# Optimization experiments

Hardware: AMD Instinct MI355X
Metric: run time of the kernel (lower is better)

The kernel has to match this reference:

```python
import jax, jax.numpy as jnp
import numpy as np

H = 16  # hidden size = time_slot(=32) / 2
G = 3 * H  # gate dim (r|z|n), torch gate order


def _gru_dir(x, Wi, Wh, bi, bh, reverse):
    """Single-direction GRU over time. x: [B,T,F]; Wi:[3H,F]; Wh:[3H,H]."""
    xp = jnp.einsum('btf,gf->btg', x, Wi) + bi  # [B,T,3H] input projections, all steps at once
    if reverse:
        xp = xp[:, ::-1]
    xp_t = jnp.swapaxes(xp, 0, 1)  # [T,B,3H]
    h0 = jnp.zeros((x.shape[0], H), x.dtype)

    def step(h, g_x):
        g_h = h @ Wh.T + bh  # [B,3H]
        r = jax.nn.sigmoid(g_x[:, :H] + g_h[:, :H])
        z = jax.nn.sigmoid(g_x[:, H:2 * H] + g_h[:, H:2 * H])
        n = jnp.tanh(g_x[:, 2 * H:] + r * g_h[:, 2 * H:])
        h_new = (1.0 - z) * n + z * h
        return h_new, h_new

    _, ys = jax.lax.scan(step, h0, xp_t)
    ys = jnp.swapaxes(ys, 0, 1)  # [B,T,H]
    if reverse:
        ys = ys[:, ::-1]
    return ys


def _bigru(x, Wi, Wh, bi, bh):
    """Bidirectional GRU layer; params indexed [dir(2), ...]."""
    fwd = _gru_dir(x, Wi[0], Wh[0], bi[0], bh[0], False)
    bwd = _gru_dir(x, Wi[1], Wh[1], bi[1], bh[1], True)
    return jnp.concatenate([fwd, bwd], axis=-1)  # [B,T,2H]


def setup_inputs() -> dict:
    key = jax.random.key(0)
    ks = jax.random.split(key, 12)
    B, T, F_IN, DEPTH, NCLS = 16384, 64, 3, 5, 4
    s = 0.25  # ~1/sqrt(H) torch init scale
    return {
        'x': jax.random.normal(ks[0], (B, T, F_IN), jnp.float32),
        # GRU1: 1 layer, 2 directions, input 3
        'Wi1': jax.random.normal(ks[1], (2, G, F_IN), jnp.float32) * s,
        'Wh1': jax.random.normal(ks[2], (2, G, H), jnp.float32) * s,
        'bi1': jax.random.normal(ks[3], (2, G), jnp.float32) * s,
        'bh1': jax.random.normal(ks[4], (2, G), jnp.float32) * s,
        # GRU5: 5 layers, 2 directions, input 2H=32 every layer
        'Wi5': jax.random.normal(ks[5], (DEPTH, 2, G, 2 * H), jnp.float32) * s,
        'Wh5': jax.random.normal(ks[6], (DEPTH, 2, G, H), jnp.float32) * s,
        'bi5': jax.random.normal(ks[7], (DEPTH, 2, G), jnp.float32) * s,
        'bh5': jax.random.normal(ks[8], (DEPTH, 2, G), jnp.float32) * s,
        # classifier Linear(2H -> num_class)
        'Wc': jax.random.normal(ks[9], (NCLS, 2 * H), jnp.float32) * s,
        'bc': jax.random.normal(ks[10], (NCLS,), jnp.float32) * s,
    }


def reference(x, Wi1, Wh1, bi1, bh1, Wi5, Wh5, bi5, bh5, Wc, bc):
    y = _bigru(x, Wi1, Wh1, bi1, bh1)  # [B,T,2H]
    for l in range(Wi5.shape[0]):  # 5 stacked bi-GRU layers
        y = _bigru(y, Wi5[l], Wh5[l], bi5[l], bh5[l])
    logits = jnp.einsum('btd,cd->btc', y, Wc) + bc  # [B,T,num_class]
    return jax.nn.softmax(logits, axis=2)
```

## Files before the change

### kernel.cpp

```cpp
#include <hip/hip_runtime.h>

#define T 64
#define F_IN 3
#define H 16
#define G 48
#define D2 32
#define DEPTH 5
#define NCLS 4
#define L2E 1.44269504f

#define YST 32
#define YSB 2048
#define HZ_ZOFF 64

typedef _Float16 half8 __attribute__((ext_vector_type(8)));
typedef float f32x4v __attribute__((ext_vector_type(4)));

__device__ __forceinline__ float fexp2(float x) { return __builtin_amdgcn_exp2f(x); }
__device__ __forceinline__ float frcp(float x)  { return __builtin_amdgcn_rcpf(x); }

__global__ __launch_bounds__(64, 3) void bigru_all(
    const float* __restrict__ x,
    const float* __restrict__ Wi1, const float* __restrict__ Wh1,
    const float* __restrict__ bi1, const float* __restrict__ bh1,
    const float* __restrict__ Wi5, const float* __restrict__ Wh5,
    const float* __restrict__ bi5, const float* __restrict__ bh5,
    const float* __restrict__ Wc,  const float* __restrict__ bc,
    float* __restrict__ out)
{
    __shared__ __align__(16) _Float16 yb[2 * YSB];
    __shared__ __align__(16) _Float16 hzb[80];
    __shared__ __align__(16) float xls[512];

    const int lane = threadIdx.x;
    const int j15  = lane & 15;
    const int quad = lane >> 4;
    const int lb   = quad & 1;
    const int dir  = quad >> 1;
    const bool isf = (dir == 0);

    hzb[lane] = (_Float16)0.0f;
    if (lane < 16) hzb[64 + lane] = (_Float16)0.0f;

    {
        const float* xg0 = x + (size_t)blockIdx.x * (2 * T * F_IN);
        #pragma unroll
        for (int k = 0; k < 2; ++k) {
            int idx = lane + 64 * k;
            float a0 = xg0[3 * idx], a1 = xg0[3 * idx + 1], a2 = xg0[3 * idx + 2];
            float4 v; v.x = a0; v.y = a1; v.z = a2; v.w = 0.0f;
            *(float4*)(xls + 4 * idx) = v;
        }
    }

    const int  job_a  = j15 >> 2;
    const bool avalid = ((j15 >> 3) == 0) ? (quad < 2) : (quad >= 2);
    const _Float16* aptr = hzb + (avalid ? (job_a * 16 + (quad & 1) * 8) : HZ_ZOFF);

    const int ystep = isf ? YST : -YST;
    const f32x4v zC = {0.f, 0.f, 0.f, 0.f};
    const int klo = (quad & 1) * 8;
    const int bdir = (quad < 2) ? 0 : 1;

    float hj;
    half8 ag = *(const half8*)aptr;

    {
        half8 whB[3];
        {
            const float* wsrc = Wh1 + bdir * (G * H);
            #pragma unroll
            for (int g = 0; g < 3; ++g) {
                const float scale = (g == 2) ? (-2.0f * L2E) : L2E;
                const float* w = wsrc + (g * 16 + j15) * H + klo;
                half8 hv;
                #pragma unroll
                for (int i = 0; i < 8; ++i) hv[i] = (_Float16)(scale * w[i]);
                whB[g] = hv;
            }
        }
        float wi[3][F_IN];
        float bir[3], bhn2;
        {
            const float* Wi = Wi1 + dir * (G * F_IN);
            const float* bi = bi1 + dir * G;
            const float* bh = bh1 + dir * G;
            #pragma unroll
            for (int g = 0; g < 3; ++g) {
                const float scale = (g == 2) ? (-2.0f * L2E) : L2E;
                int row = g * H + j15;
                #pragma unroll
                for (int k = 0; k < F_IN; ++k) wi[g][k] = scale * Wi[row * F_IN + k];
                bir[g] = scale * bi[row] + ((g < 2) ? (L2E * bh[row]) : 0.0f);
            }
            bhn2 = -2.0f * L2E * bh[2 * H + j15];
        }
        const f32x4v cN = {bhn2, bhn2, bhn2, bhn2};
        hj = 0.0f;

        int xi = lb * 64 + (isf ? 0 : (T - 1));
        const int xstep = isf ? 1 : -1;
        _Float16* yw = yb + lb * YSB + (isf ? 0 : (T - 1)) * YST + dir * H + j15;

        #pragma unroll 4
        for (int s = 0; s < T; ++s) {
            float4 xv = *(const float4*)(xls + 4 * xi);
            xi += xstep;
            float gxr = fmaf(wi[0][2], xv.z, fmaf(wi[0][1], xv.y, fmaf(wi[0][0], xv.x, bir[0])));
            float gxz = fmaf(wi[1][2], xv.z, fmaf(wi[1][1], xv.y, fmaf(wi[1][0], xv.x, bir[1])));
            float gxn = fmaf(wi[2][2], xv.z, fmaf(wi[2][1], xv.y, fmaf(wi[2][0], xv.x, bir[2])));
            f32x4v d0 = __builtin_amdgcn_mfma_f32_16x16x32_f16(ag, whB[0], zC, 0, 0, 0);
            f32x4v d1 = __builtin_amdgcn_mfma_f32_16x16x32_f16(ag, whB[1], zC, 0, 0, 0);
            f32x4v d2 = __builtin_amdgcn_mfma_f32_16x16x32_f16(ag, whB[2], cN, 0, 0, 0);
            float av = gxr + d0[0];
            float bv = gxz + d1[0];
            float Er = fexp2(-av);
            float Ez = fexp2(-bv);
            float rg = frcp(1.0f + Er);
            float c2 = fmaf(rg, d2[0], gxn);
            float Ec = fexp2(c2);
            float dz = 1.0f + Ez;
            float num = fmaf(hj - Ez, Ec, hj + Ez);
            float den = fmaf(dz, Ec, dz);
            float hn = num * frcp(den);
            hj = hn;
            _Float16 hh = (_Float16)hn;
            hzb[lane] = hh;
            ag = *(const half8*)aptr;
            *yw = hh;
            yw += ystep;
        }
    }

    #pragma unroll 1
    for (int l = 0; l < DEPTH; ++l) {
        half8 bflo[3], bfhi[3];
        #pragma unroll
        for (int g = 0; g < 3; ++g) {
            const float scale = (g == 2) ? (-2.0f * L2E) : L2E;
            const float* w = Wi5 + ((size_t)(l * 2 + bdir) * G + g * 16 + j15) * D2;
            half8 lo, hi;
            #pragma unroll
            for (int i = 0; i < 8; ++i) {
                lo[i] = (_Float16)(scale * w[klo + i]);
                hi[i] = (_Float16)(scale * w[16 + klo + i]);
            }
            bflo[g] = lo;
            bfhi[g] = hi;
        }
        half8 whB[3];
        {
            const float* wsrc = Wh5 + ((size_t)(l * 2) + bdir) * G * H;
            #pragma unroll
            for (int g = 0; g < 3; ++g) {
                const float scale = (g == 2) ? (-2.0f * L2E) : L2E;
                const float* w = wsrc + (g * 16 + j15) * H + klo;
                half8 hv;
                #pragma unroll
                for (int i = 0; i < 8; ++i) hv[i] = (_Float16)(scale * w[i]);
                whB[g] = hv;
            }
        }
        float bib0, bib1, bib2, bhn2;
        {
            const float* biL = bi5 + (l * 2 + dir) * G;
            const float* bhL = bh5 + (l * 2 + dir) * G;
            bib0 = L2E * (biL[j15]     + bhL[j15]);
            bib1 = L2E * (biL[H + j15] + bhL[H + j15]);
            bib2 = -2.0f * L2E * biL[2 * H + j15];
            bhn2 = -2.0f * L2E * bhL[2 * H + j15];
        }
        const f32x4v cR  = {bib0, bib0, bib0, bib0};
        const f32x4v cZ  = {bib1, bib1, bib1, bib1};
        const f32x4v cNx = {bib2, bib2, bib2, bib2};
        const f32x4v cN  = {bhn2, bhn2, bhn2, bhn2};

        hj = 0.0f;
        hzb[lane] = (_Float16)0.0f;
        ag = *(const half8*)aptr;

        const bool fsel = (j15 < 8);
        const int  lb_a = (j15 >> 2) & 1;
        const int  tl_a = j15 & 3;
        const bool axv  = fsel ? (quad < 2) : (quad >= 2);

        const _Float16* ap;
        int apstep, hioff;
        if (axv) {
            ap     = yb + lb_a * YSB + (fsel ? tl_a : (T - 1 - tl_a)) * YST + klo;
            apstep = fsel ? (4 * YST) : -(4 * YST);
            hioff  = 16;
        } else {
            ap     = hzb + HZ_ZOFF;
            apstep = 0;
            hioff  = 0;
        }

        unsigned int ypk[16];

        #pragma unroll
        for (int c = 0; c < 8; ++c) {
            half8 alo = *(const half8*)ap;
            half8 ahi = *(const half8*)(ap + hioff);
            ap += apstep;
            f32x4v c0 = __builtin_amdgcn_mfma_f32_16x16x32_f16(alo, bflo[0], cR, 0, 0, 0);
            f32x4v c1 = __builtin_amdgcn_mfma_f32_16x16x32_f16(alo, bflo[1], cZ, 0, 0, 0);
            f32x4v c2g = __builtin_amdgcn_mfma_f32_16x16x32_f16(alo, bflo[2], cNx, 0, 0, 0);
            c0  = __builtin_amdgcn_mfma_f32_16x16x32_f16(ahi, bfhi[0], c0, 0, 0, 0);
            c1  = __builtin_amdgcn_mfma_f32_16x16x32_f16(ahi, bfhi[1], c1, 0, 0, 0);
            c2g = __builtin_amdgcn_mfma_f32_16x16x32_f16(ahi, bfhi[2], c2g, 0, 0, 0);

            #pragma unroll
            for (int s = 0; s < 4; ++s) {
                f32x4v d0 = __builtin_amdgcn_mfma_f32_16x16x32_f16(ag, whB[0], c0, 0, 0, 0);
                f32x4v d1 = __builtin_amdgcn_mfma_f32_16x16x32_f16(ag, whB[1], c1, 0, 0, 0);
                f32x4v d2 = __builtin_amdgcn_mfma_f32_16x16x32_f16(ag, whB[2], cN, 0, 0, 0);
                float Er = fexp2(-d0[s]);
                float Ez = fexp2(-d1[s]);
                float rg = frcp(1.0f + Er);
                float cc = fmaf(rg, d2[0], c2g[s]);
                float Ec = fexp2(cc);
                float dz = 1.0f + Ez;
                float num = fmaf(hj - Ez, Ec, hj + Ez);
                float den = fmaf(dz, Ec, dz);
                float hn = num * frcp(den);
                hj = hn;
                _Float16 hh = (_Float16)hn;
                hzb[lane] = hh;
                ag = *(const half8*)aptr;
                unsigned int hb16 = (unsigned int)__builtin_bit_cast(unsigned short, hh);
                if (s & 1) ypk[2 * c + (s >> 1)] |= hb16 << 16;
                else       ypk[2 * c + (s >> 1)]  = hb16;
            }
        }

        {
            _Float16* yw = yb + lb * YSB + (isf ? 32 : 31) * YST + dir * H + j15;
            #pragma unroll 1
            for (int c = 8; c < 16; ++c) {
                half8 alo = *(const half8*)ap;
                half8 ahi = *(const half8*)(ap + hioff);
                ap += apstep;
                f32x4v c0 = __builtin_amdgcn_mfma_f32_16x16x32_f16(alo, bflo[0], cR, 0, 0, 0);
                f32x4v c1 = __builtin_amdgcn_mfma_f32_16x16x32_f16(alo, bflo[1], cZ, 0, 0, 0);
                f32x4v c2g = __builtin_amdgcn_mfma_f32_16x16x32_f16(alo, bflo[2], cNx, 0, 0, 0);
                c0  = __builtin_amdgcn_mfma_f32_16x16x32_f16(ahi, bfhi[0], c0, 0, 0, 0);
                c1  = __builtin_amdgcn_mfma_f32_16x16x32_f16(ahi, bfhi[1], c1, 0, 0, 0);
                c2g = __builtin_amdgcn_mfma_f32_16x16x32_f16(ahi, bfhi[2], c2g, 0, 0, 0);

                unsigned int w01 = 0, w23 = 0;
                #pragma unroll
                for (int s = 0; s < 4; ++s) {
                    f32x4v d0 = __builtin_amdgcn_mfma_f32_16x16x32_f16(ag, whB[0], c0, 0, 0, 0);
                    f32x4v d1 = __builtin_amdgcn_mfma_f32_16x16x32_f16(ag, whB[1], c1, 0, 0, 0);
                    f32x4v d2 = __builtin_amdgcn_mfma_f32_16x16x32_f16(ag, whB[2], cN, 0, 0, 0);
                    float Er = fexp2(-d0[s]);
                    float Ez = fexp2(-d1[s]);
                    float rg = frcp(1.0f + Er);
                    float cc = fmaf(rg, d2[0], c2g[s]);
                    float Ec = fexp2(cc);
                    float dz = 1.0f + Ez;
                    float num = fmaf(hj - Ez, Ec, hj + Ez);
                    float den = fmaf(dz, Ec, dz);
                    float hn = num * frcp(den);
                    hj = hn;
                    _Float16 hh = (_Float16)hn;
                    hzb[lane] = hh;
                    ag = *(const half8*)aptr;
                    unsigned int hb16 = (unsigned int)__builtin_bit_cast(unsigned short, hh);
                    if (s & 1) { if (s >> 1) w23 |= hb16 << 16; else w01 |= hb16 << 16; }
                    else       { if (s >> 1) w23  = hb16;       else w01  = hb16; }
                }
                *yw = __builtin_bit_cast(_Float16, (unsigned short)(w01 & 0xffffu)); yw += ystep;
                *yw = __builtin_bit_cast(_Float16, (unsigned short)(w01 >> 16));     yw += ystep;
                *yw = __builtin_bit_cast(_Float16, (unsigned short)(w23 & 0xffffu)); yw += ystep;
                *yw = __builtin_bit_cast(_Float16, (unsigned short)(w23 >> 16));     yw += ystep;
            }
        }

        {
            _Float16* yw = yb + lb * YSB + (isf ? 0 : (T - 1)) * YST + dir * H + j15;
            #pragma unroll
            for (int i = 0; i < 16; ++i) {
                unsigned int v = ypk[i];
                *yw = __builtin_bit_cast(_Float16, (unsigned short)(v & 0xffffu));
                yw += ystep;
                *yw = __builtin_bit_cast(_Float16, (unsigned short)(v >> 16));
                yw += ystep;
            }
        }
    }

    #pragma unroll
    for (int i = 0; i < 2; ++i) {
        int idx = lane + i * 64;
        int bb  = idx >> 6;
        int t   = idx & 63;
        const _Float16* yrow = yb + bb * YSB + t * YST;
        float yv[D2];
        #pragma unroll
        for (int k8 = 0; k8 < 4; ++k8) {
            half8 v = *(const half8*)(yrow + k8 * 8);
            #pragma unroll
            for (int i8 = 0; i8 < 8; ++i8) yv[k8 * 8 + i8] = (float)v[i8];
        }
        float lg[NCLS];
        #pragma unroll
        for (int c = 0; c < NCLS; ++c) {
            const float* wc = Wc + c * D2;
            float acc = bc[c];
            #pragma unroll
            for (int k = 0; k < D2; ++k) acc = fmaf(wc[k], yv[k], acc);
            lg[c] = acc;
        }
        float m = fmaxf(fmaxf(lg[0], lg[1]), fmaxf(lg[2], lg[3]));
        float e0 = __expf(lg[0] - m), e1 = __expf(lg[1] - m);
        float e2 = __expf(lg[2] - m), e3 = __expf(lg[3] - m);
        float inv = frcp(e0 + e1 + e2 + e3);
        size_t bglob = (size_t)blockIdx.x * 2 + bb;
        float4 o;
        o.x = e0 * inv; o.y = e1 * inv; o.z = e2 * inv; o.w = e3 * inv;
        ((float4*)out)[bglob * T + t] = o;
    }
}

extern "C" void kernel_launch(void* const* d_in, const int* in_sizes, int n_in,
                              void* d_out, int out_size, void* d_ws, size_t ws_size,
                              hipStream_t stream) {
    const float* x   = (const float*)d_in[0];
    const float* Wi1 = (const float*)d_in[1];
    const float* Wh1 = (const float*)d_in[2];
    const float* bi1 = (const float*)d_in[3];
    const float* bh1 = (const float*)d_in[4];
    const float* Wi5 = (const float*)d_in[5];
    const float* Wh5 = (const float*)d_in[6];
    const float* bi5 = (const float*)d_in[7];
    const float* bh5 = (const float*)d_in[8];
    const float* Wc  = (const float*)d_in[9];
    const float* bc  = (const float*)d_in[10];
    float* out = (float*)d_out;

    const int B = in_sizes[0] / (T * F_IN);
    dim3 grid(B / 2), block(64);
    hipLaunchKernelGGL(bigru_all, grid, block, 0, stream,
                       x, Wi1, Wh1, bi1, bh1, Wi5, Wh5, bi5, bh5, Wc, bc, out);
}
```

Measured before the change: 313.4 us.

## Drop separate x staging buffer by packing inputs into y buffer; raise occupancy

Removes the 2 KB xls shared array and stores the layer-1 inputs inside the unused parts of the y ping buffer, arranged so each timestep's x is read before that row is overwritten by GRU outputs. The 64-step loop is split into two 32-step halves walking the buffer in opposite directions to make the aliasing safe. Launch bounds are raised from 3 to 4 waves per SIMD so that more blocks can fit once LDS per block shrinks. The aliasing scheme is delicate: forward and backward directions write rows that must not clobber x entries that are still unread, and the higher bound may force register spills.

New measurement: 357.2 us. 14.0% more time.

```diff
diff --git a/kernel.cpp b/kernel.cpp
--- a/kernel.cpp
+++ b/kernel.cpp
@@ -19,7 +19,7 @@
 __device__ __forceinline__ float fexp2(float x) { return __builtin_amdgcn_exp2f(x); }
 __device__ __forceinline__ float frcp(float x)  { return __builtin_amdgcn_rcpf(x); }
 
-__global__ __launch_bounds__(64, 3) void bigru_all(
+__global__ __launch_bounds__(64, 4) void bigru_all(
     const float* __restrict__ x,
     const float* __restrict__ Wi1, const float* __restrict__ Wh1,
     const float* __restrict__ bi1, const float* __restrict__ bh1,
@@ -30,7 +30,6 @@
 {
     __shared__ __align__(16) _Float16 yb[2 * YSB];
     __shared__ __align__(16) _Float16 hzb[80];
-    __shared__ __align__(16) float xls[512];
 
     const int lane = threadIdx.x;
     const int j15  = lane & 15;
@@ -47,9 +46,13 @@
         #pragma unroll
         for (int k = 0; k < 2; ++k) {
             int idx = lane + 64 * k;
+            int lbx = idx >> 6;
+            int t   = idx & 63;
+            int row = (t >= 32) ? t : (63 - t);
+            int off = (t >= 32) ? 0 : 8;
             float a0 = xg0[3 * idx], a1 = xg0[3 * idx + 1], a2 = xg0[3 * idx + 2];
             float4 v; v.x = a0; v.y = a1; v.z = a2; v.w = 0.0f;
-            *(float4*)(xls + 4 * idx) = v;
+            *(float4*)(yb + lbx * YSB + row * YST + off) = v;
         }
     }
 
@@ -98,14 +101,42 @@
         const f32x4v cN = {bhn2, bhn2, bhn2, bhn2};
         hj = 0.0f;
 
-        int xi = lb * 64 + (isf ? 0 : (T - 1));
-        const int xstep = isf ? 1 : -1;
         _Float16* yw = yb + lb * YSB + (isf ? 0 : (T - 1)) * YST + dir * H + j15;
+        const _Float16* xp = yb + lb * YSB + 63 * YST + (isf ? 8 : 0);
 
         #pragma unroll 4
-        for (int s = 0; s < T; ++s) {
-            float4 xv = *(const float4*)(xls + 4 * xi);
-            xi += xstep;
+        for (int s = 0; s < 32; ++s) {
+            float4 xv = *(const float4*)xp;
+            xp -= YST;
+            float gxr = fmaf(wi[0][2], xv.z, fmaf(wi[0][1], xv.y, fmaf(wi[0][0], xv.x, bir[0])));
+            float gxz = fmaf(wi[1][2], xv.z, fmaf(wi[1][1], xv.y, fmaf(wi[1][0], xv.x, bir[1])));
+            float gxn = fmaf(wi[2][2], xv.z, fmaf(wi[2][1], xv.y, fmaf(wi[2][0], xv.x, bir[2])));
+            f32x4v d0 = __builtin_amdgcn_mfma_f32_16x16x32_f16(ag, whB[0], zC, 0, 0, 0);
+            f32x4v d1 = __builtin_amdgcn_mfma_f32_16x16x32_f16(ag, whB[1], zC, 0, 0, 0);
+            f32x4v d2 = __builtin_amdgcn_mfma_f32_16x16x32_f16(ag, whB[2], cN, 0, 0, 0);
+            float av = gxr + d0[0];
+            float bv = gxz + d1[0];
+            float Er = fexp2(-av);
+            float Ez = fexp2(-bv);
+            float rg = frcp(1.0f + Er);
+            float c2 = fmaf(rg, d2[0], gxn);
+            float Ec = fexp2(c2);
+            float dz = 1.0f + Ez;
+            float num = fmaf(hj - Ez, Ec, hj + Ez);
+            float den = fmaf(dz, Ec, dz);
+            float hn = num * frcp(den);
+            hj = hn;
+            _Float16 hh = (_Float16)hn;
+            hzb[lane] = hh;
+            ag = *(const half8*)aptr;
+            *yw = hh;
+            yw += ystep;
+        }
+        xp = yb + lb * YSB + 32 * YST + (isf ? 0 : 8);
+        #pragma unroll 4
+        for (int s = 32; s < 64; ++s) {
+            float4 xv = *(const float4*)xp;
+            xp += YST;
             float gxr = fmaf(wi[0][2], xv.z, fmaf(wi[0][1], xv.y, fmaf(wi[0][0], xv.x, bir[0])));
             float gxz = fmaf(wi[1][2], xv.z, fmaf(wi[1][1], xv.y, fmaf(wi[1][0], xv.x, bir[1])));
             float gxn = fmaf(wi[2][2], xv.z, fmaf(wi[2][1], xv.y, fmaf(wi[2][0], xv.x, bir[2])));
```
